# Optimization experiments

Hardware: AMD Instinct MI355X
Metric: run time of the kernel (lower is better)

Reference implementation:

```python
import jax, jax.numpy as jnp
import numpy as np

BN_EPS = 1e-3
EPS = 1e-8
IGNORE = -1


def _head(x, w1, b1, g, be, w2, b2):
    # Linear -> BatchNorm1d (training: batch stats, biased var) -> ReLU -> Linear
    h = x @ w1 + b1
    mu = h.mean(axis=0)
    var = h.var(axis=0)  # biased, matches torch BN normalization
    h = (h - mu) * jax.lax.rsqrt(var + BN_EPS) * g + be
    h = jax.nn.relu(h)
    return h @ w2 + b2


def _bias_losses(a, b, mask):
    # faithful to compute_loss(bias_gt, bias_pred, mask); l1 and cosine are symmetric
    dist = jnp.sum(jnp.abs(a - b), axis=-1)
    denom = jnp.sum(mask) + EPS
    l1 = jnp.sum(dist * mask) / denom
    an = a / (jnp.linalg.norm(a, axis=-1, keepdims=True) + EPS)
    bn = b / (jnp.linalg.norm(b, axis=-1, keepdims=True) + EPS)
    cos = -jnp.sum(an * bn, axis=-1)
    cl = jnp.sum(cos * mask) / denom
    return l1, cl


def setup_inputs() -> dict:
    key = jax.random.key(0)
    ks = jax.random.split(key, 12)
    N, C, S = 1048576, 64, 20
    inp = {
        'feat': jax.random.normal(ks[0], (N, C), jnp.float32),
        'coord': jax.random.normal(ks[1], (N, 3), jnp.float32) * 2.0,
        'segment': jax.random.randint(ks[2], (N,), -1, S).astype(jnp.int32),
        'instance': jax.random.randint(ks[3], (N,), -1, 200).astype(jnp.int32),
        'instance_centroid': jax.random.normal(ks[4], (N, 3), jnp.float32) * 2.0,
        'w1_xy': jax.random.normal(ks[5], (C, C), jnp.float32) * 0.05,
        'b1_xy': jnp.zeros((C,), jnp.float32),
        'g_xy': jnp.ones((C,), jnp.float32),
        'be_xy': jnp.zeros((C,), jnp.float32),
        'w2_xy': jax.random.normal(ks[6], (C, 2), jnp.float32) * 0.05,
        'b2_xy': jnp.zeros((2,), jnp.float32),
        'w1_z': jax.random.normal(ks[7], (C, C), jnp.float32) * 0.05,
        'b1_z': jnp.zeros((C,), jnp.float32),
        'g_z': jnp.ones((C,), jnp.float32),
        'be_z': jnp.zeros((C,), jnp.float32),
        'w2_z': jax.random.normal(ks[8], (C, 1), jnp.float32) * 0.05,
        'b2_z': jnp.zeros((1,), jnp.float32),
        'w_seg': jax.random.normal(ks[9], (C, S), jnp.float32) * 0.05,
        'b_seg': jnp.zeros((S,), jnp.float32),
    }
    return inp


def reference(feat, coord, segment, instance, instance_centroid,
              w1_xy, b1_xy, g_xy, be_xy, w2_xy, b2_xy,
              w1_z, b1_z, g_z, be_z, w2_z, b2_z,
              w_seg, b_seg):
    bias_pred_xy = _head(feat, w1_xy, b1_xy, g_xy, be_xy, w2_xy, b2_xy)  # [N,2]
    bias_pred_z = _head(feat, w1_z, b1_z, g_z, be_z, w2_z, b2_z)         # [N,1]
    logit_pred = feat @ w_seg + b_seg                                     # [N,S]

    # cross-entropy with ignore_index=-1, unit class weights
    valid = (segment != IGNORE)
    tgt = jnp.where(valid, segment, 0)
    logp = jax.nn.log_softmax(logit_pred, axis=-1)
    nll = -jnp.take_along_axis(logp, tgt[:, None], axis=1)[:, 0]
    vf = valid.astype(logit_pred.dtype)
    seg_loss = jnp.sum(nll * vf) / jnp.sum(vf)

    mask = (instance != IGNORE).astype(feat.dtype)
    bias_gt = instance_centroid - coord
    l1_xy, cos_xy = _bias_losses(bias_gt[:, :2], bias_pred_xy, mask)
    l1_z, cos_z = _bias_losses(bias_gt[:, 2:3], bias_pred_z, mask)

    # faithful to original (bias_xy_l1 counted twice, xy cosine unused in total)
    loss = seg_loss + l1_xy + l1_xy + 0.5 * (l1_z + cos_z)
    return (loss, seg_loss, l1_xy, cos_xy, l1_z, cos_z)
```

## Files before the change

kernel.cpp:

```cpp
#include <hip/hip_runtime.h>
#include <hip/hip_bf16.h>

#define OFF_COLSUM 0
#define OFF_S      64
#define OFF_ACC    4160
#define OFF_DONE   4168
#define OFF_ZEND   4169
#define OFF_SHX    4176
#define OFF_SHZ    4240
#define OFF_W1XS   4304
#define OFF_W1ZS   6352
#define OFF_WSEGS  8400

typedef __attribute__((ext_vector_type(8))) short bf16x8;
typedef __attribute__((ext_vector_type(4))) float f32x4;

__device__ __forceinline__ unsigned short f2bfh(float x) {
    __hip_bfloat16 h = __float2bfloat16(x);
    return *reinterpret_cast<unsigned short*>(&h);
}

union BF8 { bf16x8 v; unsigned short u[8]; };

__device__ __forceinline__ void gload_lds16(const void* g, void* l) {
    __builtin_amdgcn_global_load_lds((const __attribute__((address_space(1))) void*)g,
                                     (__attribute__((address_space(3))) void*)l, 16, 0, 0);
}


__global__ __launch_bounds__(256, 4) void k_stats(const float* __restrict__ feat,
                                                  int N, int ntiles, int tpb,
                                                  float* __restrict__ ws) {
    __shared__ __align__(16) float ftile[2][4096];
    const int t = threadIdx.x;
    const int lane = t & 63, l15 = lane & 15, grp = lane >> 4, wv = t >> 6;

    const f32x4 z4 = {0.f, 0.f, 0.f, 0.f};
    f32x4 acc[4] = {z4, z4, z4, z4};
    float csum = 0.f;

    const int l3 = l15 & 3;
    const int cb_base = l15 >> 2;
    const int g1x8 = (grp & 1) * 8;

    const int ti0 = blockIdx.x * tpb;
    const int tiend = min(ti0 + tpb, ntiles);

    auto stage = [&](int bufi, int ti) {
        const int row0 = ti * 64;
        if (row0 + 64 <= N) {
#pragma unroll
            for (int c = 0; c < 4; c++) {
                const int r = (wv * 4 + c) * 4 + grp;
                const int u = l15 ^ (r & 15);
                gload_lds16(&feat[(size_t)(row0 + r) * 64 + u * 4],
                            &ftile[bufi][(wv * 4 + c) * 256]);
            }
        } else {
#pragma unroll
            for (int u2 = 0; u2 < 4; u2++) {
                const int i = t + u2 * 256;
                const int r = i >> 4, u = (i & 15) ^ (r & 15);
                float4 v = make_float4(0.f, 0.f, 0.f, 0.f);
                if (row0 + r < N) v = *(const float4*)&feat[(size_t)(row0 + r) * 64 + u * 4];
                *(float4*)&ftile[bufi][i * 4] = v;
            }
        }
    };

    if (ti0 < tiend) stage(0, ti0);
    int cur = 0;
    for (int ti = ti0; ti < tiend; ++ti) {
        __syncthreads();
        if (ti + 1 < tiend) stage(cur ^ 1, ti + 1);
        const float* fb = ftile[cur];

        bf16x8 fr[4][2];
#pragma unroll
        for (int s = 0; s < 4; s++) {
            const int g = (wv + s) & 3;
            const int cb = (g * 4 + cb_base) ^ g1x8;
#pragma unroll
            for (int h = 0; h < 2; h++) {
                const int pbase = h * 32 + grp * 8;
                float vs[8];
#pragma unroll
                for (int kk = 0; kk < 8; kk++)
                    vs[kk] = fb[(pbase + kk) * 64 + ((cb ^ kk) << 2) + l3];
                BF8 fv;
#pragma unroll
                for (int kk = 0; kk < 8; kk++) fv.u[kk] = f2bfh(vs[kk]);
                fr[s][h] = fv.v;
                if (s == 0) {
#pragma unroll
                    for (int kk = 0; kk < 8; kk++) csum += vs[kk];
                }
            }
        }
#pragma unroll
        for (int s = 0; s < 4; s++) {
            acc[s] = __builtin_amdgcn_mfma_f32_16x16x32_bf16(fr[0][0], fr[s][0], acc[s], 0, 0, 0);
            acc[s] = __builtin_amdgcn_mfma_f32_16x16x32_bf16(fr[0][1], fr[s][1], acc[s], 0, 0, 0);
        }
        cur ^= 1;
    }

    float* S = ws + OFF_S;
#pragma unroll
    for (int s = 0; s < 4; s++) {
        const int gj = (wv + s) & 3;
#pragma unroll
        for (int r = 0; r < 4; r++)
            atomicAdd(&S[(wv * 16 + grp * 4 + r) * 64 + gj * 16 + l15], acc[s][r]);
    }
    csum += __shfl_xor(csum, 16);
    csum += __shfl_xor(csum, 32);
    if (grp == 0) atomicAdd(&ws[OFF_COLSUM + wv * 16 + l15], csum);
}

__global__ __launch_bounds__(256) void k_prep(
    const float* __restrict__ w1xy, const float* __restrict__ b1xy,
    const float* __restrict__ gxy,  const float* __restrict__ bexy,
    const float* __restrict__ w1z,  const float* __restrict__ b1z,
    const float* __restrict__ gz,   const float* __restrict__ bez,
    const float* __restrict__ wseg, float Nf, float* __restrict__ ws) {
    __shared__ float S[64][64];
    __shared__ float cs[64];
    const int t = threadIdx.x;

    for (int i = t; i < 4096; i += 256) ((float*)S)[i] = ws[OFF_S + i];
    if (t < 64) cs[t] = ws[OFF_COLSUM + t];
    __syncthreads();

    if (t < 128) {
        const int head = t >> 6, j = t & 63;
        const float* w1 = head ? w1z : w1xy;
        float w[64];
#pragma unroll
        for (int k = 0; k < 64; k++) w[k] = w1[k * 64 + j];
        float d = 0.f;
#pragma unroll
        for (int k = 0; k < 64; k++) d = fmaf(cs[k], w[k], d);
        float quad = 0.f;
#pragma unroll
        for (int k = 0; k < 64; k++) {
            float rd = 0.f;
#pragma unroll
            for (int l = 0; l < 64; l++) rd = fmaf(S[k][l], w[l], rd);
            quad = fmaf(w[k], rd, quad);
        }
        const float b1 = head ? b1z[j] : b1xy[j];
        const float mu  = d / Nf + b1;
        const float eh2 = quad / Nf + 2.f * b1 * d / Nf + b1 * b1;
        const float var = eh2 - mu * mu;
        const float g  = head ? gz[j]  : gxy[j];
        const float be = head ? bez[j] : bexy[j];
        const float sc = g * rsqrtf(var + 1e-3f);
        const float sh = be - mu * sc;
        ws[(head ? OFF_SHZ : OFF_SHX) + j] = sh;
        unsigned short* dst = (unsigned short*)(ws + (head ? OFF_W1ZS : OFF_W1XS));
#pragma unroll
        for (int k = 0; k < 64; k++) dst[j * 64 + k] = f2bfh(w[k] * sc);
    } else if (t < 160) {
        const int j = t - 128;
        unsigned short* dst = (unsigned short*)(ws + OFF_WSEGS);
        for (int k = 0; k < 64; k++)
            dst[j * 64 + k] = (j < 20) ? f2bfh(wseg[k * 20 + j]) : (unsigned short)0;
    }
}

__global__ __launch_bounds__(256, 2) void k_loss(
    const float* __restrict__ feat, const float* __restrict__ coord,
    const int* __restrict__ seg, const int* __restrict__ inst,
    const float* __restrict__ cent,
    const unsigned short* __restrict__ w1xs, const unsigned short* __restrict__ w1zs,
    const unsigned short* __restrict__ wsegs,
    const float* __restrict__ shxv, const float* __restrict__ shzv,
    const float* __restrict__ w2xy, const float* __restrict__ b2xy,
    const float* __restrict__ w2z,  const float* __restrict__ b2z,
    const float* __restrict__ bseg,
    int N, int ntiles, int tpb, float* __restrict__ acc, float* __restrict__ out) {
    __shared__ __align__(16) float ftile[2][4096];
    __shared__ float red[4][8];

    const int t = threadIdx.x;
    const int lane = t & 63, l15 = lane & 15, grp = lane >> 4, wv = t >> 6;

    bf16x8 ax[4][2], az[4][2], ag[2][2];
#pragma unroll
    for (int nt = 0; nt < 4; nt++)
#pragma unroll
        for (int h = 0; h < 2; h++) {
            ax[nt][h] = *(const bf16x8*)&w1xs[(nt * 16 + l15) * 64 + grp * 8 + h * 32];
            az[nt][h] = *(const bf16x8*)&w1zs[(nt * 16 + l15) * 64 + grp * 8 + h * 32];
        }
#pragma unroll
    for (int nt = 0; nt < 2; nt++)
#pragma unroll
        for (int h = 0; h < 2; h++)
            ag[nt][h] = *(const bf16x8*)&wsegs[(nt * 16 + l15) * 64 + grp * 8 + h * 32];

    float shx_c[4][4], shz_c[4][4], w20[4][4], w21[4][4], w2zc[4][4], bs_c[2][4];
#pragma unroll
    for (int nt = 0; nt < 4; nt++)
#pragma unroll
        for (int r = 0; r < 4; r++) {
            const int c = nt * 16 + grp * 4 + r;
            shx_c[nt][r] = shxv[c]; shz_c[nt][r] = shzv[c];
            w20[nt][r] = w2xy[c * 2]; w21[nt][r] = w2xy[c * 2 + 1];
            w2zc[nt][r] = w2z[c];
        }
#pragma unroll
    for (int nt = 0; nt < 2; nt++)
#pragma unroll
        for (int r = 0; r < 4; r++) {
            const int c = nt * 16 + grp * 4 + r;
            bs_c[nt][r] = (c < 20) ? bseg[c] : -1e30f;
        }
    const float pb0 = b2xy[0], pb1 = b2xy[1], pbz = b2z[0];

    float s_nll = 0.f, s_vf = 0.f, s_l1xy = 0.f, s_cosxy = 0.f;
    float s_l1z = 0.f, s_cosz = 0.f, s_mask = 0.f;

    const int ti0 = blockIdx.x * tpb;
    const int tiend = min(ti0 + tpb, ntiles);

    auto stage = [&](int bufi, int ti) {
        const int row0 = ti * 64;
        if (row0 + 64 <= N) {
#pragma unroll
            for (int c = 0; c < 4; c++) {
                const int r = (wv * 4 + c) * 4 + grp;
                const int u = l15 ^ (r & 15);
                gload_lds16(&feat[(size_t)(row0 + r) * 64 + u * 4],
                            &ftile[bufi][(wv * 4 + c) * 256]);
            }
        } else {
#pragma unroll
            for (int u2 = 0; u2 < 4; u2++) {
                const int i = t + u2 * 256;
                const int r = i >> 4, u = (i & 15) ^ (r & 15);
                float4 v = make_float4(0.f, 0.f, 0.f, 0.f);
                if (row0 + r < N) v = *(const float4*)&feat[(size_t)(row0 + r) * 64 + u * 4];
                *(float4*)&ftile[bufi][i * 4] = v;
            }
        }
    };

    int p_tg = -1, p_iv = -1;
    float p_c0 = 0.f, p_c1 = 0.f, p_c2 = 0.f, p_e0 = 0.f, p_e1 = 0.f, p_e2 = 0.f;
    auto ptload = [&](int ti) {
        const int gp = ti * 64 + wv * 16 + l15;
        const bool inb = (gp < N);
        p_tg = inb ? seg[gp] : -1;
        p_iv = inb ? inst[gp] : -1;
        if (inb) {
            p_c0 = coord[(size_t)gp * 3]; p_c1 = coord[(size_t)gp * 3 + 1]; p_c2 = coord[(size_t)gp * 3 + 2];
            p_e0 = cent[(size_t)gp * 3];  p_e1 = cent[(size_t)gp * 3 + 1];  p_e2 = cent[(size_t)gp * 3 + 2];
        } else {
            p_c0 = p_c1 = p_c2 = p_e0 = p_e1 = p_e2 = 0.f;
        }
    };

    if (ti0 < tiend) { stage(0, ti0); ptload(ti0); }
    int cur = 0;
    for (int ti = ti0; ti < tiend; ++ti) {
        const int tg = p_tg, iv = p_iv;
        const float c0 = p_c0, c1 = p_c1, c2 = p_c2, e0 = p_e0, e1 = p_e1, e2 = p_e2;

        __syncthreads();
        if (ti + 1 < tiend) { stage(cur ^ 1, ti + 1); ptload(ti + 1); }

        const int p = wv * 16 + l15;
        const float* fb = ftile[cur];
        const float4 q0 = *(const float4*)&fb[(p * 16 + ((grp * 2)     ^ l15)) * 4];
        const float4 q1 = *(const float4*)&fb[(p * 16 + ((grp * 2 + 1) ^ l15)) * 4];
        const float4 q2 = *(const float4*)&fb[(p * 16 + ((8 + grp * 2) ^ l15)) * 4];
        const float4 q3 = *(const float4*)&fb[(p * 16 + ((9 + grp * 2) ^ l15)) * 4];
        BF8 b0, b1;
        b0.u[0] = f2bfh(q0.x); b0.u[1] = f2bfh(q0.y); b0.u[2] = f2bfh(q0.z); b0.u[3] = f2bfh(q0.w);
        b0.u[4] = f2bfh(q1.x); b0.u[5] = f2bfh(q1.y); b0.u[6] = f2bfh(q1.z); b0.u[7] = f2bfh(q1.w);
        b1.u[0] = f2bfh(q2.x); b1.u[1] = f2bfh(q2.y); b1.u[2] = f2bfh(q2.z); b1.u[3] = f2bfh(q2.w);
        b1.u[4] = f2bfh(q3.x); b1.u[5] = f2bfh(q3.y); b1.u[6] = f2bfh(q3.z); b1.u[7] = f2bfh(q3.w);

        f32x4 cg0 = {bs_c[0][0], bs_c[0][1], bs_c[0][2], bs_c[0][3]};
        cg0 = __builtin_amdgcn_mfma_f32_16x16x32_bf16(ag[0][0], b0.v, cg0, 0, 0, 0);
        cg0 = __builtin_amdgcn_mfma_f32_16x16x32_bf16(ag[0][1], b1.v, cg0, 0, 0, 0);
        f32x4 cg1 = {bs_c[1][0], bs_c[1][1], bs_c[1][2], bs_c[1][3]};
        cg1 = __builtin_amdgcn_mfma_f32_16x16x32_bf16(ag[1][0], b0.v, cg1, 0, 0, 0);
        cg1 = __builtin_amdgcn_mfma_f32_16x16x32_bf16(ag[1][1], b1.v, cg1, 0, 0, 0);
        float lmax = cg0[0];
#pragma unroll
        for (int r = 1; r < 4; r++) lmax = fmaxf(lmax, cg0[r]);
#pragma unroll
        for (int r = 0; r < 4; r++) lmax = fmaxf(lmax, cg1[r]);
        lmax = fmaxf(lmax, __shfl_xor(lmax, 16));
        lmax = fmaxf(lmax, __shfl_xor(lmax, 32));
        float se = 0.f;
#pragma unroll
        for (int r = 0; r < 4; r++) se += __expf(cg0[r] - lmax);
#pragma unroll
        for (int r = 0; r < 4; r++) se += __expf(cg1[r] - lmax);
        se += __shfl_xor(se, 16); se += __shfl_xor(se, 32);
        const float lse = lmax + __logf(se);
        float lt = 0.f;
#pragma unroll
        for (int r = 0; r < 4; r++) lt += (grp * 4 + r == tg) ? cg0[r] : 0.f;
#pragma unroll
        for (int r = 0; r < 4; r++) lt += (16 + grp * 4 + r == tg) ? cg1[r] : 0.f;
        lt += __shfl_xor(lt, 16); lt += __shfl_xor(lt, 32);
        const float vf = (tg >= 0) ? 1.f : 0.f;
        s_nll += (lse - lt) * vf;
        s_vf += vf;

        float s0 = 0.f, s1 = 0.f, szv = 0.f;
#pragma unroll
        for (int nt = 0; nt < 4; nt++) {
            f32x4 cc = {shx_c[nt][0], shx_c[nt][1], shx_c[nt][2], shx_c[nt][3]};
            cc = __builtin_amdgcn_mfma_f32_16x16x32_bf16(ax[nt][0], b0.v, cc, 0, 0, 0);
            cc = __builtin_amdgcn_mfma_f32_16x16x32_bf16(ax[nt][1], b1.v, cc, 0, 0, 0);
#pragma unroll
            for (int r = 0; r < 4; r++) {
                const float hx = fmaxf(cc[r], 0.f);
                s0 = fmaf(hx, w20[nt][r], s0);
                s1 = fmaf(hx, w21[nt][r], s1);
            }
            f32x4 cz = {shz_c[nt][0], shz_c[nt][1], shz_c[nt][2], shz_c[nt][3]};
            cz = __builtin_amdgcn_mfma_f32_16x16x32_bf16(az[nt][0], b0.v, cz, 0, 0, 0);
            cz = __builtin_amdgcn_mfma_f32_16x16x32_bf16(az[nt][1], b1.v, cz, 0, 0, 0);
#pragma unroll
            for (int r = 0; r < 4; r++) {
                const float hz = fmaxf(cz[r], 0.f);
                szv = fmaf(hz, w2zc[nt][r], szv);
            }
        }
        s0 += __shfl_xor(s0, 16);  s0 += __shfl_xor(s0, 32);
        s1 += __shfl_xor(s1, 16);  s1 += __shfl_xor(s1, 32);
        szv += __shfl_xor(szv, 16); szv += __shfl_xor(szv, 32);
        const float p0 = s0 + pb0, p1 = s1 + pb1, pz = szv + pbz;

        const float mk = (iv >= 0) ? 1.f : 0.f;
        const float a0 = e0 - c0, a1 = e1 - c1, a2 = e2 - c2;
        s_l1xy += (fabsf(a0 - p0) + fabsf(a1 - p1)) * mk;
        const float na = sqrtf(a0 * a0 + a1 * a1) + 1e-8f;
        const float nb = sqrtf(p0 * p0 + p1 * p1) + 1e-8f;
        s_cosxy -= ((a0 * p0 + a1 * p1) / (na * nb)) * mk;
        s_l1z += fabsf(a2 - pz) * mk;
        const float naz = fabsf(a2) + 1e-8f, nbz = fabsf(pz) + 1e-8f;
        s_cosz -= ((a2 * pz) / (naz * nbz)) * mk;
        s_mask += mk;

        cur ^= 1;
    }

    float v[7] = {s_nll * 0.25f, s_vf * 0.25f, s_l1xy * 0.25f, s_cosxy * 0.25f,
                  s_l1z * 0.25f, s_cosz * 0.25f, s_mask * 0.25f};
#pragma unroll
    for (int i = 0; i < 7; i++) {
#pragma unroll
        for (int o = 32; o > 0; o >>= 1) v[i] += __shfl_down(v[i], o);
    }
    if (lane == 0) {
#pragma unroll
        for (int i = 0; i < 7; i++) red[wv][i] = v[i];
    }
    __syncthreads();
    if (t < 7) {
        float s = red[0][t] + red[1][t] + red[2][t] + red[3][t];
        atomicAdd(&acc[t], s);
    }
    __syncthreads();
    if (t == 0) {
        __threadfence();
        int* done = (int*)(acc + (OFF_DONE - OFF_ACC));
        if (atomicAdd(done, 1) == (int)gridDim.x - 1) {
            __threadfence();
            float sv[7];
#pragma unroll
            for (int i = 0; i < 7; i++) sv[i] = atomicAdd(&acc[i], 0.f);
            const float segl = sv[0] / sv[1];
            const float den = sv[6] + 1e-8f;
            const float l1xy = sv[2] / den, cosxy = sv[3] / den;
            const float l1z = sv[4] / den, cosz = sv[5] / den;
            out[0] = segl + l1xy + l1xy + 0.5f * (l1z + cosz);
            out[1] = segl;
            out[2] = l1xy;
            out[3] = cosxy;
            out[4] = l1z;
            out[5] = cosz;
        }
    }
}

extern "C" void kernel_launch(void* const* d_in, const int* in_sizes, int n_in,
                              void* d_out, int out_size, void* d_ws, size_t ws_size,
                              hipStream_t stream) {
    const float* feat  = (const float*)d_in[0];
    const float* coord = (const float*)d_in[1];
    const int*   segm  = (const int*)d_in[2];
    const int*   inst  = (const int*)d_in[3];
    const float* cent  = (const float*)d_in[4];
    const float* w1xy  = (const float*)d_in[5];
    const float* b1xy  = (const float*)d_in[6];
    const float* gxy   = (const float*)d_in[7];
    const float* bexy  = (const float*)d_in[8];
    const float* w2xy  = (const float*)d_in[9];
    const float* b2xy  = (const float*)d_in[10];
    const float* w1z   = (const float*)d_in[11];
    const float* b1z   = (const float*)d_in[12];
    const float* gz    = (const float*)d_in[13];
    const float* bez   = (const float*)d_in[14];
    const float* w2z   = (const float*)d_in[15];
    const float* b2z   = (const float*)d_in[16];
    const float* wseg  = (const float*)d_in[17];
    const float* bseg  = (const float*)d_in[18];

    const int N = in_sizes[0] / 64;
    float* ws = (float*)d_ws;
    const int ntiles = (N + 63) >> 6;

    const int grid_s = 1024;
    const int tpb_s = (ntiles + grid_s - 1) / grid_s;
    const int grid_l = 512;
    const int tpb_l = (ntiles + grid_l - 1) / grid_l;

    hipMemsetAsync(d_ws, 0, OFF_ZEND * sizeof(float), stream);

    k_stats<<<grid_s, 256, 0, stream>>>(feat, N, ntiles, tpb_s, ws);
    k_prep<<<1, 256, 0, stream>>>(w1xy, b1xy, gxy, bexy, w1z, b1z, gz, bez, wseg,
                                  (float)N, ws);
    k_loss<<<grid_l, 256, 0, stream>>>(
        feat, coord, segm, inst, cent,
        (const unsigned short*)(ws + OFF_W1XS),
        (const unsigned short*)(ws + OFF_W1ZS),
        (const unsigned short*)(ws + OFF_WSEGS),
        ws + OFF_SHX, ws + OFF_SHZ,
        w2xy, b2xy, w2z, b2z, bseg, N, ntiles, tpb_l,
        ws + OFF_ACC, (float*)d_out);
}
```

Measured before the change: 195.8 us.

## Convert feat tiles to bf16 once in LDS and deepen stats pipeline

Result: slower. 757.0 us (+286.7%).

```diff
diff --git a/kernel.cpp b/kernel.cpp
--- a/kernel.cpp
+++ b/kernel.cpp
@@ -28,20 +28,36 @@
 }
 
 
-__global__ __launch_bounds__(256, 4) void k_stats(const float* __restrict__ feat,
+__global__ __launch_bounds__(256, 3) void k_stats(const float* __restrict__ feat,
                                                   int N, int ntiles, int tpb,
                                                   float* __restrict__ ws) {
-    __shared__ __align__(16) float ftile[2][4096];
+    __shared__ __align__(16) float f32t[2][4096];
+    __shared__ __align__(16) unsigned int bft[2][64 * 36];
     const int t = threadIdx.x;
     const int lane = t & 63, l15 = lane & 15, grp = lane >> 4, wv = t >> 6;
+    const int o = t & 7;
+    const int pp = t >> 3;
 
     const f32x4 z4 = {0.f, 0.f, 0.f, 0.f};
     f32x4 acc[4] = {z4, z4, z4, z4};
-    float csum = 0.f;
-
-    const int l3 = l15 & 3;
-    const int cb_base = l15 >> 2;
-    const int g1x8 = (grp & 1) * 8;
+    float cs[8] = {0.f, 0.f, 0.f, 0.f, 0.f, 0.f, 0.f, 0.f};
+
+    int roff[4][2];
+#pragma unroll
+    for (int s = 0; s < 4; s++) {
+        const int g = (wv + s) & 3;
+        const int ch = g * 16 + l15;
+        const int ob = ch >> 3;
+#pragma unroll
+        for (int h = 0; h < 2; h++)
+            roff[s][h] = ch * 36 + ((h * 16 + grp * 4) ^ (4 * ob));
+    }
+    const int r0 = 2 * pp, r1 = 2 * pp + 1;
+    const int u00 = r0 * 16 + ((2 * o)     ^ (r0 & 15));
+    const int u01 = r0 * 16 + ((2 * o + 1) ^ (r0 & 15));
+    const int u10 = r1 * 16 + ((2 * o)     ^ (r1 & 15));
+    const int u11 = r1 * 16 + ((2 * o + 1) ^ (r1 & 15));
+    const int wbase = (8 * o) * 36 + (pp ^ (4 * o));
 
     const int ti0 = blockIdx.x * tpb;
     const int tiend = min(ti0 + tpb, ntiles);
@@ -54,7 +70,7 @@
                 const int r = (wv * 4 + c) * 4 + grp;
                 const int u = l15 ^ (r & 15);
                 gload_lds16(&feat[(size_t)(row0 + r) * 64 + u * 4],
-                            &ftile[bufi][(wv * 4 + c) * 256]);
+                            &f32t[bufi][(wv * 4 + c) * 256]);
             }
         } else {
 #pragma unroll
@@ -63,46 +79,48 @@
                 const int r = i >> 4, u = (i & 15) ^ (r & 15);
                 float4 v = make_float4(0.f, 0.f, 0.f, 0.f);
                 if (row0 + r < N) v = *(const float4*)&feat[(size_t)(row0 + r) * 64 + u * 4];
-                *(float4*)&ftile[bufi][i * 4] = v;
+                *(float4*)&f32t[bufi][i * 4] = v;
             }
         }
     };
 
+    auto convert = [&](int b) {
+        const float4 a0 = *(const float4*)&f32t[b][u00 * 4];
+        const float4 a1 = *(const float4*)&f32t[b][u01 * 4];
+        const float4 c0 = *(const float4*)&f32t[b][u10 * 4];
+        const float4 c1 = *(const float4*)&f32t[b][u11 * 4];
+        const float lo[8] = {a0.x, a0.y, a0.z, a0.w, a1.x, a1.y, a1.z, a1.w};
+        const float hi[8] = {c0.x, c0.y, c0.z, c0.w, c1.x, c1.y, c1.z, c1.w};
+#pragma unroll
+        for (int c = 0; c < 8; c++) {
+            cs[c] += lo[c] + hi[c];
+            bft[b][wbase + c * 36] =
+                (unsigned)f2bfh(lo[c]) | ((unsigned)f2bfh(hi[c]) << 16);
+        }
+    };
+
     if (ti0 < tiend) stage(0, ti0);
-    int cur = 0;
-    for (int ti = ti0; ti < tiend; ++ti) {
+    __syncthreads();
+    if (ti0 < tiend) convert(0);
+    if (ti0 + 1 < tiend) stage(1, ti0 + 1);
+
+    for (int i = ti0; i < tiend; ++i) {
+        const int ib = i & 1;
         __syncthreads();
-        if (ti + 1 < tiend) stage(cur ^ 1, ti + 1);
-        const float* fb = ftile[cur];
+        if (i + 2 < tiend) stage(ib, i + 2);
+        if (i + 1 < tiend) convert(ib ^ 1);
 
         bf16x8 fr[4][2];
 #pragma unroll
-        for (int s = 0; s < 4; s++) {
-            const int g = (wv + s) & 3;
-            const int cb = (g * 4 + cb_base) ^ g1x8;
-#pragma unroll
-            for (int h = 0; h < 2; h++) {
-                const int pbase = h * 32 + grp * 8;
-                float vs[8];
-#pragma unroll
-                for (int kk = 0; kk < 8; kk++)
-                    vs[kk] = fb[(pbase + kk) * 64 + ((cb ^ kk) << 2) + l3];
-                BF8 fv;
-#pragma unroll
-                for (int kk = 0; kk < 8; kk++) fv.u[kk] = f2bfh(vs[kk]);
-                fr[s][h] = fv.v;
-                if (s == 0) {
-#pragma unroll
-                    for (int kk = 0; kk < 8; kk++) csum += vs[kk];
-                }
-            }
-        }
+        for (int s = 0; s < 4; s++)
+#pragma unroll
+            for (int h = 0; h < 2; h++)
+                fr[s][h] = *(const bf16x8*)&bft[ib][roff[s][h]];
 #pragma unroll
         for (int s = 0; s < 4; s++) {
             acc[s] = __builtin_amdgcn_mfma_f32_16x16x32_bf16(fr[0][0], fr[s][0], acc[s], 0, 0, 0);
             acc[s] = __builtin_amdgcn_mfma_f32_16x16x32_bf16(fr[0][1], fr[s][1], acc[s], 0, 0, 0);
         }
-        cur ^= 1;
     }
 
     float* S = ws + OFF_S;
@@ -113,9 +131,12 @@
         for (int r = 0; r < 4; r++)
             atomicAdd(&S[(wv * 16 + grp * 4 + r) * 64 + gj * 16 + l15], acc[s][r]);
     }
-    csum += __shfl_xor(csum, 16);
-    csum += __shfl_xor(csum, 32);
-    if (grp == 0) atomicAdd(&ws[OFF_COLSUM + wv * 16 + l15], csum);
+#pragma unroll
+    for (int c = 0; c < 8; c++) {
+        float v = cs[c];
+        v += __shfl_xor(v, 8); v += __shfl_xor(v, 16); v += __shfl_xor(v, 32);
+        if ((lane >> 3) == 0) atomicAdd(&ws[OFF_COLSUM + 8 * o + c], v);
+    }
 }
 
 __global__ __launch_bounds__(256) void k_prep(
@@ -419,7 +440,7 @@
     float* ws = (float*)d_ws;
     const int ntiles = (N + 63) >> 6;
 
-    const int grid_s = 1024;
+    const int grid_s = 768;
     const int tpb_s = (ntiles + grid_s - 1) / grid_s;
     const int grid_l = 512;
     const int tpb_l = (ntiles + grid_l - 1) / grid_l;
```
